# Optimization experiments

Measured on AMD Instinct MI355X. Metric: run time of the kernel, lower is better.

Reference implementation:

```python
import jax, jax.numpy as jnp
import numpy as np

NA = 50000
NB = 50000
E = 800000
D = 256


def setup_inputs() -> dict:
    key = jax.random.key(0)
    ks = jax.random.split(key, 7)
    feature_a = jax.random.normal(ks[0], (NA, D), dtype=jnp.float32)
    feature_b = jax.random.normal(ks[1], (NB, D), dtype=jnp.float32)
    # Linear(b_dim, b_dim): store weight pre-transposed so new_emb = feature_b @ W + b
    W = jax.random.normal(ks[2], (D, D), dtype=jnp.float32) * (1.0 / np.sqrt(D))
    b = jnp.zeros((D,), dtype=jnp.float32)
    # kaiming-normal-ish init for attention vector a: [a_dim + b_dim, 1]
    a = jax.random.normal(ks[3], (2 * D, 1), dtype=jnp.float32) * np.sqrt(2.0 / (2 * D))
    edge_src = jnp.sort(jax.random.randint(ks[4], (E,), 0, NA, dtype=jnp.int32)).astype(jnp.int64)
    edge_dst = jax.random.randint(ks[5], (E,), 0, NB, dtype=jnp.int64)
    return {
        "feature_a": feature_a,
        "feature_b": feature_b,
        "W": W,
        "b": b,
        "a": a,
        "edge_src": edge_src,
        "edge_dst": edge_dst,
        "node_num_a": NA,
        "node_num_b": NB,
    }


def reference(feature_a, feature_b, W, b, a, edge_src, edge_dst, node_num_a, node_num_b):
    # new_emb = out_mlp_layer(feature_b)
    new_emb = feature_b @ W + b  # [Nb, D]

    # cat([feature_a[src], new_emb[dst]]) @ a  ==  (feature_a @ a_top)[src] + (new_emb @ a_bot)[dst]
    a_dim = feature_a.shape[1]
    a_top = a[:a_dim, 0]   # [a_dim]
    a_bot = a[a_dim:, 0]   # [b_dim]
    s_a = feature_a @ a_top   # [Na]
    s_b = new_emb @ a_bot     # [Nb]
    logits = s_a[edge_src] + s_b[edge_dst]  # [E]

    # exp(elu(x, alpha=0.1))
    elu = jnp.where(logits > 0, logits, 0.1 * jnp.expm1(logits))
    score = jnp.exp(elu)  # [E]

    # sparse mm: weighted aggregation of new_emb over edges, grouped by src
    msg = score[:, None] * new_emb[edge_dst]  # [E, D]
    agg = jax.ops.segment_sum(msg, edge_src, num_segments=node_num_a)       # [Na, D]
    row_sum = jax.ops.segment_sum(score, edge_src, num_segments=node_num_a)  # [Na]
    row_sum = jnp.where(row_sum == 0, 1.0, row_sum)[:, None]
    return agg / row_sum
```

## Files before the change

### kernel.cpp

```cpp
#include <hip/hip_runtime.h>
#include <cstdint>

#define NA_N 50000
#define NB_N 50000
#define NE_N 800000
#define DD 256

using bf8   = __attribute__((ext_vector_type(8))) short;
using f32x4 = __attribute__((ext_vector_type(4))) float;
using u16x8 = __attribute__((ext_vector_type(8))) ushort;

__device__ __forceinline__ ushort f2bf(float f) {
    uint u = __float_as_uint(f);
    uint r = (u + 0x7fffu + ((u >> 16) & 1u)) >> 16;
    return (ushort)r;
}
__device__ __forceinline__ float bf2f(ushort u) {
    return __uint_as_float(((uint)u) << 16);
}

__global__ __launch_bounds__(256) void wt_cast(const float* __restrict__ W,
                                               ushort* __restrict__ Wt)
{
    __shared__ float T[64][65];
    const int bi = blockIdx.x & 3;
    const int bj = blockIdx.x >> 2;
    const int lane = threadIdx.x & 63, w = threadIdx.x >> 6;
    for (int i = w; i < 64; i += 4)
        T[i][lane] = W[(size_t)(bi * 64 + i) * DD + bj * 64 + lane];
    __syncthreads();
    for (int i = w; i < 64; i += 4)
        Wt[(size_t)(bj * 64 + i) * DD + bi * 64 + lane] = f2bf(T[lane][i]);
}

__global__ __launch_bounds__(256) void gemm_mfma(
    const float* __restrict__ A, const ushort* __restrict__ Wt,
    const float* __restrict__ bias, const float* __restrict__ a_bot,
    ushort* __restrict__ C, float* __restrict__ s_b)
{
    __shared__ ushort As[64 * 264];
    __shared__ float  sdot[4][64];
    const int t  = threadIdx.x;
    const int r0 = blockIdx.x * 64;

#pragma unroll
    for (int i = 0; i < 16; i++) {
        int flat = i * 256 + t;
        int row  = flat >> 6;
        int c4   = flat & 63;
        int gr   = r0 + row; if (gr >= NB_N) gr = 0;
        float4 v = ((const float4*)(A + (size_t)gr * DD))[c4];
        ushort4 b;
        b.x = f2bf(v.x); b.y = f2bf(v.y); b.z = f2bf(v.z); b.w = f2bf(v.w);
        *(ushort4*)&As[row * 264 + c4 * 4] = b;
    }
    __syncthreads();

    const int lane = t & 63;
    const int wv   = t >> 6;
    const int lr   = lane & 15;
    const int lk   = (lane >> 4) * 8;

    f32x4 acc[4][4];
#pragma unroll
    for (int m = 0; m < 4; m++)
#pragma unroll
        for (int n = 0; n < 4; n++) acc[m][n] = (f32x4){0.f, 0.f, 0.f, 0.f};

#pragma unroll
    for (int ks = 0; ks < 8; ks++) {
        const int k0 = ks * 32;
        bf8 af[4], bb[4];
#pragma unroll
        for (int m = 0; m < 4; m++)
            af[m] = *(const bf8*)&As[(m * 16 + lr) * 264 + k0 + lk];
#pragma unroll
        for (int n = 0; n < 4; n++) {
            int col = wv * 64 + n * 16 + lr;
            bb[n] = *(const bf8*)&Wt[(size_t)col * DD + k0 + lk];
        }
#pragma unroll
        for (int m = 0; m < 4; m++)
#pragma unroll
            for (int n = 0; n < 4; n++)
                acc[m][n] = __builtin_amdgcn_mfma_f32_16x16x32_bf16(
                    af[m], bb[n], acc[m][n], 0, 0, 0);
    }

    float abv[4];
#pragma unroll
    for (int n = 0; n < 4; n++) abv[n] = a_bot[wv * 64 + n * 16 + lr];

    float part[4][4];
#pragma unroll
    for (int m = 0; m < 4; m++)
#pragma unroll
        for (int r = 0; r < 4; r++) part[m][r] = 0.f;

#pragma unroll
    for (int m = 0; m < 4; m++)
#pragma unroll
        for (int n = 0; n < 4; n++) {
            int   col = wv * 64 + n * 16 + lr;
            float bv  = bias[col];
#pragma unroll
            for (int r = 0; r < 4; r++) {
                int   rowg = r0 + m * 16 + (lane >> 4) * 4 + r;
                float v    = acc[m][n][r] + bv;
                if (rowg < NB_N) C[(size_t)rowg * DD + col] = f2bf(v);
                part[m][r] = fmaf(v, abv[n], part[m][r]);
            }
        }

#pragma unroll
    for (int m = 0; m < 4; m++)
#pragma unroll
        for (int r = 0; r < 4; r++) {
#pragma unroll
            for (int off = 1; off < 16; off <<= 1)
                part[m][r] += __shfl_xor(part[m][r], off, 64);
        }
    if (lr == 0) {
#pragma unroll
        for (int m = 0; m < 4; m++)
#pragma unroll
            for (int r = 0; r < 4; r++)
                sdot[wv][m * 16 + (lane >> 4) * 4 + r] = part[m][r];
    }
    __syncthreads();
    if (t < 64) {
        int rowg = r0 + t;
        if (rowg < NB_N)
            s_b[rowg] = sdot[0][t] + sdot[1][t] + sdot[2][t] + sdot[3][t];
    }
}

__global__ void rowstart_k(const int* __restrict__ esrc, int* __restrict__ row_start)
{
    int e = blockIdx.x * 256 + threadIdx.x;
    if (e >= NE_N) return;
    int s    = esrc[e];
    int prev = (e == 0) ? -1 : esrc[e - 1];
    for (int r = prev + 1; r <= s; r++) row_start[r] = e;
    if (e == NE_N - 1)
        for (int r = s + 1; r <= NA_N; r++) row_start[r] = NE_N;
}

__global__ __launch_bounds__(256) void edge_agg4(
    const int* __restrict__ edst, const int* __restrict__ row_start,
    const float* __restrict__ fa, const float* __restrict__ a_top,
    const float* __restrict__ sb, const ushort* __restrict__ emb,
    float* __restrict__ out)
{
    const int lane = threadIdx.x & 63;
    const int a    = blockIdx.x * 4 + (threadIdx.x >> 6);
    if (a >= NA_N) return;

    float4 av = ((const float4*)(fa + (size_t)a * DD))[lane];
    float4 tv = ((const float4*)a_top)[lane];
    float  sa_a = av.x * tv.x + av.y * tv.y + av.z * tv.z + av.w * tv.w;
#pragma unroll
    for (int off = 1; off < 64; off <<= 1) sa_a += __shfl_xor(sa_a, off, 64);

    const int g = lane >> 4;
    const int c = lane & 15;
    const int beg = row_start[a], end = row_start[a + 1];

    float accA[8], accB[8];
#pragma unroll
    for (int j = 0; j < 8; j++) { accA[j] = 0.f; accB[j] = 0.f; }
    float rs = 0.f;

    for (int e = beg; e < end; e += 4) {
        const int ee = e + g;
        if (ee < end) {
            int   dd = edst[ee];
            float lg = sa_a + sb[dd];
            float el = lg > 0.f ? lg : 0.1f * (__expf(lg) - 1.f);
            float s  = __expf(el);
            const ushort* rp = emb + (size_t)dd * DD + c * 16;
            u16x8 u0 = *(const u16x8*)rp;
            u16x8 u1 = *(const u16x8*)(rp + 8);
#pragma unroll
            for (int j = 0; j < 8; j++) {
                accA[j] = fmaf(s, bf2f(u0[j]), accA[j]);
                accB[j] = fmaf(s, bf2f(u1[j]), accB[j]);
            }
            rs += s;
        }
    }

#pragma unroll
    for (int j = 0; j < 8; j++) {
        accA[j] += __shfl_xor(accA[j], 16, 64);
        accA[j] += __shfl_xor(accA[j], 32, 64);
        accB[j] += __shfl_xor(accB[j], 16, 64);
        accB[j] += __shfl_xor(accB[j], 32, 64);
    }
    rs += __shfl_xor(rs, 16, 64);
    rs += __shfl_xor(rs, 32, 64);

    if (g == 0) {
        const float inv = (rs == 0.f) ? 1.f : (1.f / rs);
        float* op = out + (size_t)a * DD + c * 16;
        float4 o0 = { accA[0] * inv, accA[1] * inv, accA[2] * inv, accA[3] * inv };
        float4 o1 = { accA[4] * inv, accA[5] * inv, accA[6] * inv, accA[7] * inv };
        float4 o2 = { accB[0] * inv, accB[1] * inv, accB[2] * inv, accB[3] * inv };
        float4 o3 = { accB[4] * inv, accB[5] * inv, accB[6] * inv, accB[7] * inv };
        *(float4*)(op + 0)  = o0;
        *(float4*)(op + 4)  = o1;
        *(float4*)(op + 8)  = o2;
        *(float4*)(op + 12) = o3;
    }
}

extern "C" void kernel_launch(void* const* d_in, const int* in_sizes, int n_in,
                              void* d_out, int out_size, void* d_ws, size_t ws_size,
                              hipStream_t stream)
{
    const float* fa   = (const float*)d_in[0];
    const float* fb   = (const float*)d_in[1];
    const float* W    = (const float*)d_in[2];
    const float* bias = (const float*)d_in[3];
    const float* avec = (const float*)d_in[4];
    const int*   esrc = (const int*)d_in[5];
    const int*   edst = (const int*)d_in[6];
    float*       out  = (float*)d_out;

    char*   ws        = (char*)d_ws;
    ushort* emb_b     = (ushort*)ws;
    float*  s_b       = (float*)(ws + (size_t)NB_N * DD * 2);
    int*    row_start = (int*)(s_b + NB_N);
    ushort* Wt        = (ushort*)(row_start + NA_N + 2);

    wt_cast   <<<16, 256, 0, stream>>>(W, Wt);
    gemm_mfma <<<(NB_N + 63) / 64, 256, 0, stream>>>(fb, Wt, bias, avec + DD,
                                                     emb_b, s_b);
    rowstart_k<<<(NE_N + 255) / 256, 256, 0, stream>>>(esrc, row_start);
    edge_agg4 <<<(NA_N + 3) / 4, 256, 0, stream>>>(edst, row_start, fa, avec,
                                                   s_b, emb_b, out);
}
```

Before: 112.3 us.

## Merge weight cast with row-start build and software-pipeline edge gathers

Folds the weight transpose/cast kernel and the CSR row-start kernel into a single launch, removing one kernel launch and its serialization gap. The edge aggregation loop now prefetches the next edge's destination index, s_b value and bf16 embedding row one iteration ahead, and loads the index two iterations ahead. This is meant to hide gather latency. Out-of-range lanes are clamped to the last edge and given zero weight, which adds a few redundant loads and more register pressure.

```diff
diff --git a/kernel.cpp b/kernel.cpp
--- a/kernel.cpp
+++ b/kernel.cpp
@@ -19,18 +19,29 @@
     return __uint_as_float(((uint)u) << 16);
 }
 
-__global__ __launch_bounds__(256) void wt_cast(const float* __restrict__ W,
-                                               ushort* __restrict__ Wt)
-{
-    __shared__ float T[64][65];
-    const int bi = blockIdx.x & 3;
-    const int bj = blockIdx.x >> 2;
-    const int lane = threadIdx.x & 63, w = threadIdx.x >> 6;
-    for (int i = w; i < 64; i += 4)
-        T[i][lane] = W[(size_t)(bi * 64 + i) * DD + bj * 64 + lane];
-    __syncthreads();
-    for (int i = w; i < 64; i += 4)
-        Wt[(size_t)(bj * 64 + i) * DD + bi * 64 + lane] = f2bf(T[lane][i]);
+__global__ __launch_bounds__(256) void prep_k(const float* __restrict__ W,
+    ushort* __restrict__ Wt, const int* __restrict__ esrc,
+    int* __restrict__ row_start)
+{
+    if (blockIdx.x < 16) {
+        __shared__ float T[64][65];
+        const int bi = blockIdx.x & 3;
+        const int bj = blockIdx.x >> 2;
+        const int lane = threadIdx.x & 63, w = threadIdx.x >> 6;
+        for (int i = w; i < 64; i += 4)
+            T[i][lane] = W[(size_t)(bi * 64 + i) * DD + bj * 64 + lane];
+        __syncthreads();
+        for (int i = w; i < 64; i += 4)
+            Wt[(size_t)(bj * 64 + i) * DD + bi * 64 + lane] = f2bf(T[lane][i]);
+    } else {
+        int e = (blockIdx.x - 16) * 256 + threadIdx.x;
+        if (e >= NE_N) return;
+        int s    = esrc[e];
+        int prev = (e == 0) ? -1 : esrc[e - 1];
+        for (int r = prev + 1; r <= s; r++) row_start[r] = e;
+        if (e == NE_N - 1)
+            for (int r = s + 1; r <= NA_N; r++) row_start[r] = NE_N;
+    }
 }
 
 __global__ __launch_bounds__(256) void gemm_mfma(
@@ -135,18 +146,7 @@
     }
 }
 
-__global__ void rowstart_k(const int* __restrict__ esrc, int* __restrict__ row_start)
-{
-    int e = blockIdx.x * 256 + threadIdx.x;
-    if (e >= NE_N) return;
-    int s    = esrc[e];
-    int prev = (e == 0) ? -1 : esrc[e - 1];
-    for (int r = prev + 1; r <= s; r++) row_start[r] = e;
-    if (e == NE_N - 1)
-        for (int r = s + 1; r <= NA_N; r++) row_start[r] = NE_N;
-}
-
-__global__ __launch_bounds__(256) void edge_agg4(
+__global__ __launch_bounds__(256) void edge_agg6(
     const int* __restrict__ edst, const int* __restrict__ row_start,
     const float* __restrict__ fa, const float* __restrict__ a_top,
     const float* __restrict__ sb, const ushort* __restrict__ emb,
@@ -171,22 +171,42 @@
     for (int j = 0; j < 8; j++) { accA[j] = 0.f; accB[j] = 0.f; }
     float rs = 0.f;
 
-    for (int e = beg; e < end; e += 4) {
-        const int ee = e + g;
-        if (ee < end) {
-            int   dd = edst[ee];
-            float lg = sa_a + sb[dd];
+    if (beg < end) {
+        const int last = end - 1;
+
+        int   pc  = beg + g;
+        int   pn  = pc + 4;
+        int   dc  = edst[min(pc, last)];
+        int   dn  = edst[min(pn, last)];
+        float sbc = sb[dc];
+        float sbn = sb[dn];
+        const ushort* rc = emb + (size_t)dc * DD + c * 16;
+        u16x8 ua = *(const u16x8*)rc;
+        u16x8 ub = *(const u16x8*)(rc + 8);
+
+#pragma unroll 2
+        for (int e = beg; e < end; e += 4) {
+            const ushort* rn = emb + (size_t)dn * DD + c * 16;
+            u16x8 na = *(const u16x8*)rn;
+            u16x8 nb = *(const u16x8*)(rn + 8);
+            int   p2  = pn + 4;
+            int   d2  = edst[min(p2, last)];
+            float sb2 = sb[d2];
+
+            float lg = sa_a + sbc;
             float el = lg > 0.f ? lg : 0.1f * (__expf(lg) - 1.f);
-            float s  = __expf(el);
-            const ushort* rp = emb + (size_t)dd * DD + c * 16;
-            u16x8 u0 = *(const u16x8*)rp;
-            u16x8 u1 = *(const u16x8*)(rp + 8);
+            float s  = (pc < end) ? __expf(el) : 0.f;
+
 #pragma unroll
             for (int j = 0; j < 8; j++) {
-                accA[j] = fmaf(s, bf2f(u0[j]), accA[j]);
-                accB[j] = fmaf(s, bf2f(u1[j]), accB[j]);
+                accA[j] = fmaf(s, bf2f(ua[j]), accA[j]);
+                accB[j] = fmaf(s, bf2f(ub[j]), accB[j]);
             }
             rs += s;
+
+            pc = pn;  dc = dn;  sbc = sbn;
+            ua = na;  ub = nb;
+            pn = p2;  dn = d2;  sbn = sb2;
         }
     }
 
@@ -233,10 +253,9 @@
     int*    row_start = (int*)(s_b + NB_N);
     ushort* Wt        = (ushort*)(row_start + NA_N + 2);
 
-    wt_cast   <<<16, 256, 0, stream>>>(W, Wt);
-    gemm_mfma <<<(NB_N + 63) / 64, 256, 0, stream>>>(fb, Wt, bias, avec + DD,
-                                                     emb_b, s_b);
-    rowstart_k<<<(NE_N + 255) / 256, 256, 0, stream>>>(esrc, row_start);
-    edge_agg4 <<<(NA_N + 3) / 4, 256, 0, stream>>>(edst, row_start, fa, avec,
-                                                   s_b, emb_b, out);
-}
+    prep_k   <<<16 + (NE_N + 255) / 256, 256, 0, stream>>>(W, Wt, esrc, row_start);
+    gemm_mfma<<<(NB_N + 63) / 64, 256, 0, stream>>>(fb, Wt, bias, avec + DD,
+                                                    emb_b, s_b);
+    edge_agg6<<<(NA_N + 3) / 4, 256, 0, stream>>>(edst, row_start, fa, avec,
+                                                  s_b, emb_b, out);
+}
```

Result: faster. 108.5 us (-3.4%).
